# Performance work log

Hardware: AMD Instinct MI355X
Metric: run time of the kernel (lower is better)

## Reference

```python
import jax, jax.numpy as jnp
import numpy as np

B, C, N, K, O = 8, 64, 4096, 20, 64
BN_EPS = 1e-5
NEG_SLOPE = 0.2


def setup_inputs() -> dict:
    key = jax.random.key(0)
    k1, k2 = jax.random.split(key, 2)
    x = jax.random.normal(k1, (B, C, N), dtype=jnp.float32)
    W = jax.random.normal(k2, (O, 2 * C), dtype=jnp.float32) * 0.05  # Conv2d 1x1, no bias
    gamma = jnp.ones((O,), dtype=jnp.float32)
    beta = jnp.zeros((O,), dtype=jnp.float32)
    return {"x": x, "W": W, "gamma": gamma, "beta": beta, "k": K}


def reference(x, W, gamma, beta, k):
    # x: [B, C, N]
    xt = jnp.swapaxes(x, 1, 2)                      # [B, N, C]
    # pairwise squared distances: ||xi||^2 + ||xj||^2 - 2 xi.xj
    inner = jnp.einsum('bnc,bmc->bnm', xt, xt)      # [B, N, N]
    xx = jnp.sum(xt * xt, axis=-1)                  # [B, N]
    dist = xx[:, :, None] + xx[:, None, :] - 2.0 * inner
    # k smallest distances -> neighbor indices
    _, idx = jax.lax.top_k(-dist, k)                # [B, N, k]
    # gather neighbor features
    x_g = jax.vmap(lambda t, i: t[i])(xt, idx)      # [B, N, k, C]
    x_rep = jnp.broadcast_to(xt[:, :, None, :], x_g.shape)
    edge = jnp.concatenate([x_g - x_rep, x_rep], axis=-1)  # [B, N, k, 2C]
    # 1x1 conv == channel matmul
    h = jnp.einsum('bnkc,oc->bnko', edge, W)        # [B, N, k, O]
    # BatchNorm2d (training mode: batch statistics, biased variance)
    mean = jnp.mean(h, axis=(0, 1, 2))
    var = jnp.var(h, axis=(0, 1, 2))
    hn = (h - mean) * jax.lax.rsqrt(var + BN_EPS) * gamma + beta
    act = jnp.where(hn >= 0, hn, NEG_SLOPE * hn)    # LeakyReLU(0.2)
    out = jnp.max(act, axis=2)                      # max over k -> [B, N, O]
    return jnp.swapaxes(out, 1, 2)                  # [B, O, N]
```

## Files before the change

### kernel.cpp

```cpp
#include <hip/hip_runtime.h>
#include <hip/hip_bf16.h>

#define B_ 8
#define C_ 64
#define N_ 4096
#define K_ 20
#define O_ 64

typedef unsigned short ushort_t;
typedef __attribute__((ext_vector_type(8))) short bf16x8;
typedef __attribute__((ext_vector_type(16))) float f32x16;

constexpr float BN_EPS = 1e-5f;
constexpr float NEG = 0.2f;
constexpr int ROWS = B_ * N_;
constexpr int M_TOT = ROWS * K_;

__device__ __forceinline__ float readlane_f(float v, int src) {
  return __int_as_float(__builtin_amdgcn_readlane(__float_as_int(v), src));
}

__device__ __forceinline__ unsigned int bf16_rne(float v) {
  unsigned int u = __float_as_uint(v);
  return (u + 0x7FFFu + ((u >> 16) & 1u)) >> 16;
}


__global__ __launch_bounds__(256) void prep_kernel(const float* __restrict__ x,
                                                   const float* __restrict__ W,
                                                   float* __restrict__ y,
                                                   float* __restrict__ z,
                                                   float* __restrict__ xx,
                                                   ushort_t* __restrict__ xfh,
                                                   ushort_t* __restrict__ xfl,
                                                   ushort_t* __restrict__ xfq) {
  __shared__ float xt[64][65];
  __shared__ float w1[64][65];
  __shared__ float wd[64][65];
  const int b = blockIdx.x >> 6;
  const int n0 = (blockIdx.x & 63) << 6;
  const int tid = threadIdx.x;

  for (int rep = 0; rep < 16; ++rep) {
    int id = rep * 256 + tid;
    int cc = id >> 6, nl = id & 63;
    xt[nl][cc] = x[((b * 64 + cc) << 12) + n0 + nl];
    int o = cc, c = nl;
    float a = W[o * 128 + c];
    float bb = W[o * 128 + 64 + c];
    w1[o][c] = a;
    wd[o][c] = bb - a;
  }
  __syncthreads();

  const int o = tid & 63;
  for (int nl = tid >> 6; nl < 64; nl += 4) {
    float ay = 0.f, az = 0.f;
#pragma unroll 8
    for (int c = 0; c < 64; ++c) {
      float v = xt[nl][c];
      ay = fmaf(v, w1[o][c], ay);
      az = fmaf(v, wd[o][c], az);
    }
    int gi = (((b << 12) + n0 + nl) << 6) + o;
    y[gi] = ay;
    z[gi] = az;
  }
  if (tid < 64) {
    float s = 0.f;
#pragma unroll 8
    for (int c = 0; c < 64; ++c) {
      float v = xt[tid][c];
      s = fmaf(v, v, s);
    }
    xx[(b << 12) + tid + n0] = s;
  }

  for (int rep = 0; rep < 16; ++rep) {
    int id = rep * 256 + tid;
    int nl = id >> 6, c = id & 63;
    float v = xt[nl][c];
    unsigned int hb = bf16_rne(v);
    float hf = __uint_as_float(hb << 16);
    float r1 = v - hf;
    unsigned int lb = bf16_rne(r1);
    float lf = __uint_as_float(lb << 16);
    unsigned int qb = bf16_rne(r1 - lf);
    const int n = n0 + nl;
    const size_t addr = ((size_t)((b << 7) + (n >> 5))) * 2048
                        + ((c >> 3) << 8)
                        + ((n & 31) << 3)
                        + (c & 7);
    xfh[addr] = (ushort_t)hb;
    xfl[addr] = (ushort_t)lb;
    xfq[addr] = (ushort_t)qb;
  }
}

__global__ __launch_bounds__(512, 2) void knn_kernel(const ushort_t* __restrict__ xfh,
                                                     const ushort_t* __restrict__ xfl,
                                                     const ushort_t* __restrict__ xfq,
                                                     const float* __restrict__ xx,
                                                     int* __restrict__ idx) {
  const int tid = threadIdx.x;
  const int w = tid >> 6;
  const int lane = tid & 63;
  const int wg = ((blockIdx.x & 7) << 7) | (blockIdx.x >> 3);
  const int b = wg >> 7;
  const int i0 = (wg & 127) << 5;
  const int mcol = lane & 31;
  const int half = lane >> 5;

  __shared__ float Dld[2][32 * 256];

  const size_t atile = ((size_t)wg) * 2048;
  bf16x8 Ah[4], Al[4], Aq[4];
#pragma unroll
  for (int cc = 0; cc < 4; ++cc) {
    const size_t off = atile + (cc << 9) + (lane << 3);
    Ah[cc] = *(const bf16x8*)(xfh + off);
    Al[cc] = *(const bf16x8*)(xfl + off);
    Aq[cc] = *(const bf16x8*)(xfq + off);
  }

  float bv[4], T[4];
  int bi[4];
#pragma unroll
  for (int r = 0; r < 4; ++r) {
    bv[r] = __builtin_inff();
    T[r] = __builtin_inff();
    bi[r] = 0;
  }

  const float* xxb = xx + (b << 12);

  for (int t = 0; t < 16; ++t) {
    const int jb = t << 8;
    float* Db = Dld[t & 1];
    const size_t btile = ((size_t)((b << 7) + (t << 3) + w)) * 2048;
    f32x16 acc;
#pragma unroll
    for (int q = 0; q < 16; ++q) acc[q] = 0.f;
#pragma unroll
    for (int cc = 0; cc < 4; ++cc) {
      const size_t off = btile + (cc << 9) + (lane << 3);
      bf16x8 Bh = *(const bf16x8*)(xfh + off);
      bf16x8 Bl = *(const bf16x8*)(xfl + off);
      bf16x8 Bq = *(const bf16x8*)(xfq + off);
      acc = __builtin_amdgcn_mfma_f32_32x32x16_bf16(Ah[cc], Bh, acc, 0, 0, 0);
      acc = __builtin_amdgcn_mfma_f32_32x32x16_bf16(Ah[cc], Bl, acc, 0, 0, 0);
      acc = __builtin_amdgcn_mfma_f32_32x32x16_bf16(Al[cc], Bh, acc, 0, 0, 0);
      acc = __builtin_amdgcn_mfma_f32_32x32x16_bf16(Ah[cc], Bq, acc, 0, 0, 0);
      acc = __builtin_amdgcn_mfma_f32_32x32x16_bf16(Aq[cc], Bh, acc, 0, 0, 0);
      acc = __builtin_amdgcn_mfma_f32_32x32x16_bf16(Al[cc], Bl, acc, 0, 0, 0);
    }
    const float xxv = xxb[jb + (w << 5) + mcol];
#pragma unroll
    for (int q = 0; q < 16; ++q) {
      int row = (q & 3) + ((q >> 2) << 3) + (half << 2);
      Db[(row << 8) + (w << 5) + mcol] = fmaf(-2.f, acc[q], xxv);
    }
    __syncthreads();

#pragma unroll
    for (int r = 0; r < 4; ++r) {
      const int row = (w << 2) + r;
#pragma unroll
      for (int seg = 0; seg < 4; ++seg) {
        float v = Db[(row << 8) + (seg << 6) + lane];
        int jlane = jb + (seg << 6) + lane;
        unsigned long long rem = 0xFFFFFFFFFFFFFFFFull;
        while (true) {
          unsigned long long m = __ballot(v < T[r]) & rem;
          if (!m) break;
          int src = __ffsll(m) - 1;
          rem &= ~(1ull << src);
          float cv = readlane_f(v, src);
          int cj = __builtin_amdgcn_readlane(jlane, src);
          unsigned long long le = __ballot(bv[r] <= cv) & 0xFFFFFull;
          int pos = __popcll(le);
          float pv = __shfl_up(bv[r], 1);
          int pi = __shfl_up(bi[r], 1);
          if (lane >= pos) {
            bool ins = (lane == pos);
            bv[r] = ins ? cv : pv;
            bi[r] = ins ? cj : pi;
          }
          T[r] = readlane_f(bv[r], K_ - 1);
        }
      }
    }
  }

#pragma unroll
  for (int r = 0; r < 4; ++r) {
    if (lane < K_) idx[((b << 12) + i0 + (w << 2) + r) * K_ + lane] = bi[r];
  }
}

__global__ __launch_bounds__(256) void stats_kernel(const float* __restrict__ y,
                                                    const float* __restrict__ z,
                                                    const int* __restrict__ idx,
                                                    float* __restrict__ s1,
                                                    float* __restrict__ s2,
                                                    float* __restrict__ hmax,
                                                    float* __restrict__ hmin) {
  const int tid = threadIdx.x;
  const int o = tid & 63;
  const int r = tid >> 6;
  const int wg = ((blockIdx.x & 7) << 6) | (blockIdx.x >> 3);
  const int row0 = wg << 6;
  float a1 = 0.f, a2 = 0.f;
  for (int rl = r; rl < 64; rl += 4) {
    const int row = row0 + rl;
    const int b = row >> 12;
    const float zv = z[(row << 6) + o];
    const int* ip = idx + row * K_;
    const float* yb = y + ((size_t)b << 18);
    float s1r = 0.f;
    float hmx = -__builtin_inff();
    float hmn = __builtin_inff();
#pragma unroll
    for (int k = 0; k < K_; ++k) {
      int j = ip[k];
      float h = yb[(j << 6) + o] + zv;
      s1r += h;
      a2 = fmaf(h, h, a2);
      hmx = fmaxf(hmx, h);
      hmn = fminf(hmn, h);
    }
    a1 += s1r;
    hmax[(row << 6) + o] = hmx;
    hmin[(row << 6) + o] = hmn;
  }
  __shared__ float r1[4][64];
  __shared__ float r2[4][64];
  r1[r][o] = a1;
  r2[r][o] = a2;
  __syncthreads();
  if (tid < 64) {
    float t1 = r1[0][tid] + r1[1][tid] + r1[2][tid] + r1[3][tid];
    float t2 = r2[0][tid] + r2[1][tid] + r2[2][tid] + r2[3][tid];
    atomicAdd(&s1[tid], t1);
    atomicAdd(&s2[tid], t2);
  }
}

__global__ __launch_bounds__(256) void out_kernel(const float* __restrict__ hmax,
                                                  const float* __restrict__ hmin,
                                                  const float* __restrict__ s1,
                                                  const float* __restrict__ s2,
                                                  const float* __restrict__ gamma,
                                                  const float* __restrict__ beta,
                                                  float* __restrict__ out) {
  __shared__ float til[64][65];
  const int tid = threadIdx.x;
  const int b = blockIdx.x >> 6;
  const int n0 = (blockIdx.x & 63) << 6;
  const int o = tid & 63;
  const float mean = s1[o] / (float)M_TOT;
  const float var = s2[o] / (float)M_TOT - mean * mean;
  const float inv = 1.0f / sqrtf(var + BN_EPS);
  const float s = gamma[o] * inv;
  const float t = beta[o] - mean * s;
  const float* __restrict__ hsrc = (s >= 0.f) ? hmax : hmin;

  for (int nl = tid >> 6; nl < 64; nl += 4) {
    const int row = (b << 12) + n0 + nl;
    const float h = hsrc[(row << 6) + o];
    const float hn = fmaf(h, s, t);
    til[o][nl] = hn >= 0.f ? hn : NEG * hn;
  }
  __syncthreads();
  for (int rep = 0; rep < 16; ++rep) {
    int id = rep * 256 + tid;
    int oo = id >> 6, nl = id & 63;
    out[((size_t)((b << 6) + oo) << 12) + n0 + nl] = til[oo][nl];
  }
}

extern "C" void kernel_launch(void* const* d_in, const int* in_sizes, int n_in,
                              void* d_out, int out_size, void* d_ws, size_t ws_size,
                              hipStream_t stream) {
  const float* x = (const float*)d_in[0];
  const float* W = (const float*)d_in[1];
  const float* gamma = (const float*)d_in[2];
  const float* beta = (const float*)d_in[3];
  float* ws = (float*)d_ws;
  float* y = ws;
  float* z = ws + 2097152;
  float* xx = ws + 4194304;
  int* idxp = (int*)(ws + 4227072);
  float* s1 = ws + 4882432;
  float* s2 = ws + 4882496;
  ushort_t* xfh = (ushort_t*)(ws + 4882688);
  ushort_t* xfl = (ushort_t*)(ws + 5931264);
  ushort_t* xfq = (ushort_t*)(ws + 6979840);
  float* hmax = ws + 4882688;
  float* hmin = ws + 6979840;
  float* out = (float*)d_out;

  hipMemsetAsync(s1, 0, 2 * 64 * sizeof(float), stream);

  prep_kernel<<<512, 256, 0, stream>>>(x, W, y, z, xx, xfh, xfl, xfq);
  knn_kernel<<<ROWS / 32, 512, 0, stream>>>(xfh, xfl, xfq, xx, idxp);
  stats_kernel<<<512, 256, 0, stream>>>(y, z, idxp, s1, s2, hmax, hmin);
  out_kernel<<<512, 256, 0, stream>>>(hmax, hmin, s1, s2, gamma, beta, out);
}
```

Baseline: 415.6 us.

## Split wave into two half-waves each maintaining its own row's top-k list

The k-NN selection now has each 64-lane wave handle two query rows at once, with each 32-lane half owning one row's sorted top-20 list and scanning 32 candidates per segment. Every iteration of the insertion loop serves one candidate for each half together, which is meant to cut the serial ballot/readlane/shuffle iterations per row. The cost is a longer chain per iteration and wasted work whenever one half has no candidate while the other does, along with more segment iterations per row.

Result: slower. 461.6 us (+11.1%).

```diff
diff --git a/kernel.cpp b/kernel.cpp
--- a/kernel.cpp
+++ b/kernel.cpp
@@ -110,6 +110,7 @@
   const int i0 = (wg & 127) << 5;
   const int mcol = lane & 31;
   const int half = lane >> 5;
+  const int ln = lane & 31;
 
   __shared__ float Dld[2][32 * 256];
 
@@ -123,13 +124,13 @@
     Aq[cc] = *(const bf16x8*)(xfq + off);
   }
 
-  float bv[4], T[4];
-  int bi[4];
-#pragma unroll
-  for (int r = 0; r < 4; ++r) {
-    bv[r] = __builtin_inff();
-    T[r] = __builtin_inff();
-    bi[r] = 0;
+  float bvp[2], Tp[2];
+  int bip[2];
+#pragma unroll
+  for (int p = 0; p < 2; ++p) {
+    bvp[p] = __builtin_inff();
+    Tp[p] = __builtin_inff();
+    bip[p] = 0;
   }
 
   const float* xxb = xx + (b << 12);
@@ -163,38 +164,51 @@
     __syncthreads();
 
 #pragma unroll
-    for (int r = 0; r < 4; ++r) {
-      const int row = (w << 2) + r;
-#pragma unroll
-      for (int seg = 0; seg < 4; ++seg) {
-        float v = Db[(row << 8) + (seg << 6) + lane];
-        int jlane = jb + (seg << 6) + lane;
-        unsigned long long rem = 0xFFFFFFFFFFFFFFFFull;
+    for (int p = 0; p < 2; ++p) {
+      const int rowh = (w << 2) + (p << 1) + half;
+#pragma unroll
+      for (int seg = 0; seg < 8; ++seg) {
+        float v = Db[(rowh << 8) + (seg << 5) + ln];
+        const int jl = jb + (seg << 5) + ln;
+        unsigned int remA = ~0u, remB = ~0u;
         while (true) {
-          unsigned long long m = __ballot(v < T[r]) & rem;
-          if (!m) break;
-          int src = __ffsll(m) - 1;
-          rem &= ~(1ull << src);
-          float cv = readlane_f(v, src);
-          int cj = __builtin_amdgcn_readlane(jlane, src);
-          unsigned long long le = __ballot(bv[r] <= cv) & 0xFFFFFull;
-          int pos = __popcll(le);
-          float pv = __shfl_up(bv[r], 1);
-          int pi = __shfl_up(bi[r], 1);
-          if (lane >= pos) {
-            bool ins = (lane == pos);
-            bv[r] = ins ? cv : pv;
-            bi[r] = ins ? cj : pi;
+          const unsigned long long m64 = __ballot(v < Tp[p]);
+          const unsigned int mA = (unsigned int)(m64 & 0xFFFFFFFFull) & remA;
+          const unsigned int mB = (unsigned int)(m64 >> 32) & remB;
+          if (!(mA | mB)) break;
+          const int srcA = mA ? __builtin_ctz(mA) : 0;
+          const int srcB = mB ? __builtin_ctz(mB) : 0;
+          if (mA) remA &= ~(1u << srcA);
+          if (mB) remB &= ~(1u << srcB);
+          const float cvA = readlane_f(v, srcA);
+          const float cvB = readlane_f(v, srcB | 32);
+          const int cjA = __builtin_amdgcn_readlane(jl, srcA);
+          const int cjB = __builtin_amdgcn_readlane(jl, srcB | 32);
+          const float cv = half ? (mB ? cvB : __builtin_inff())
+                                : (mA ? cvA : __builtin_inff());
+          const int cj = half ? cjB : cjA;
+          const unsigned long long le = __ballot(bvp[p] <= cv);
+          const int pos = half ? __popcll(le & 0x000FFFFF00000000ull)
+                               : __popcll(le & 0x00000000000FFFFFull);
+          const float pv = __shfl_up(bvp[p], 1, 32);
+          const int pi = __shfl_up(bip[p], 1, 32);
+          if (ln >= pos) {
+            const bool ins = (ln == pos);
+            bvp[p] = ins ? cv : pv;
+            bip[p] = ins ? cj : pi;
           }
-          T[r] = readlane_f(bv[r], K_ - 1);
+          const float TA = readlane_f(bvp[p], 19);
+          const float TB = readlane_f(bvp[p], 51);
+          Tp[p] = half ? TB : TA;
         }
       }
     }
   }
 
 #pragma unroll
-  for (int r = 0; r < 4; ++r) {
-    if (lane < K_) idx[((b << 12) + i0 + (w << 2) + r) * K_ + lane] = bi[r];
+  for (int p = 0; p < 2; ++p) {
+    const int row = (w << 2) + (p << 1) + half;
+    if (ln < K_) idx[((b << 12) + i0 + row) * K_ + ln] = bip[p];
   }
 }
 
```
